# Kernel optimization log

Hardware: AMD Instinct MI355X
Metric: run time of the kernel (lower is better)

Reference implementation:

```python
import jax, jax.numpy as jnp
import numpy as np

B, L, D_MODEL = 4, 2048, 512
N_HEAD, D_K, D_V = 8, 64, 64
RANK = 20


def tt_linear(x, g1, g2, g3, g4, b):
    # TT-matrix linear: input modes (4,4,8,4), output modes (4,4,8,4), ranks [1,20,20,20,1]
    Bx, Lx, _ = x.shape
    t = x.reshape(Bx * Lx, 4, 4, 8, 4)
    t = jnp.einsum('bwxyz,wou->bxyzou', t, g1[0])        # g1: [1,m1,n1,r1]
    t = jnp.einsum('bxyzou,uxpv->byzopv', t, g2)         # g2: [r1,m2,n2,r2]
    t = jnp.einsum('byzopv,vyqw->bzopqw', t, g3)         # g3: [r2,m3,n3,r3]
    t = jnp.einsum('bzopqw,wzs->bopqs', t, g4[..., 0])   # g4: [r3,m4,n4,1]
    return t.reshape(Bx, Lx, -1) + b


def setup_inputs() -> dict:
    key = jax.random.key(0)
    ks = jax.random.split(key, 8)
    scale = jnp.float32(0.15)
    inp = {}
    for name, kk in zip(['wq', 'wk', 'wv', 'fc'], ks[:4]):
        sub = jax.random.split(kk, 4)
        inp[name + '_g1'] = jax.random.normal(sub[0], (1, 4, 4, RANK), jnp.float32) * scale
        inp[name + '_g2'] = jax.random.normal(sub[1], (RANK, 4, 4, RANK), jnp.float32) * scale
        inp[name + '_g3'] = jax.random.normal(sub[2], (RANK, 8, 8, RANK), jnp.float32) * scale
        inp[name + '_g4'] = jax.random.normal(sub[3], (RANK, 4, 4, 1), jnp.float32) * scale
        inp[name + '_b'] = jnp.zeros((D_MODEL,), jnp.float32)
    inp['q'] = jax.random.normal(ks[4], (B, L, D_MODEL), jnp.float32)
    inp['k'] = jax.random.normal(ks[5], (B, L, D_MODEL), jnp.float32)
    inp['v'] = jax.random.normal(ks[6], (B, L, D_MODEL), jnp.float32)
    inp['ln_g'] = jnp.ones((D_MODEL,), jnp.float32)
    inp['ln_b'] = jnp.zeros((D_MODEL,), jnp.float32)
    return inp


def reference(q, k, v,
              wq_g1, wq_g2, wq_g3, wq_g4, wq_b,
              wk_g1, wk_g2, wk_g3, wk_g4, wk_b,
              wv_g1, wv_g2, wv_g3, wv_g4, wv_b,
              fc_g1, fc_g2, fc_g3, fc_g4, fc_b,
              ln_g, ln_b):
    Bx, Lq, _ = q.shape
    residual = q
    qh = tt_linear(q, wq_g1, wq_g2, wq_g3, wq_g4, wq_b).reshape(Bx, Lq, N_HEAD, D_K).transpose(0, 2, 1, 3)
    kh = tt_linear(k, wk_g1, wk_g2, wk_g3, wk_g4, wk_b).reshape(Bx, Lq, N_HEAD, D_K).transpose(0, 2, 1, 3)
    vh = tt_linear(v, wv_g1, wv_g2, wv_g3, wv_g4, wv_b).reshape(Bx, Lq, N_HEAD, D_V).transpose(0, 2, 1, 3)
    temp = jnp.sqrt(jnp.float32(D_K))
    attn = jnp.einsum('bhqd,bhkd->bhqk', qh / temp, kh)  # explicit [B,H,L,L] scores
    attn = jax.nn.softmax(attn, axis=-1)
    o = jnp.einsum('bhqk,bhkd->bhqd', attn, vh)
    o = o.transpose(0, 2, 1, 3).reshape(Bx, Lq, N_HEAD * D_V)
    out = tt_linear(o, fc_g1, fc_g2, fc_g3, fc_g4, fc_b) + residual
    mu = out.mean(-1, keepdims=True)
    var = out.var(-1, keepdims=True)
    out = (out - mu) / jnp.sqrt(var + 1e-12) * ln_g + ln_b
    return (out, attn)
```

## Files before the change

kernel.cpp:

```cpp
#include <hip/hip_runtime.h>
#include <hip/hip_bf16.h>
#include <math.h>

#define BB 4
#define LL 2048
#define DM 512
#define NH 8
#define DK 64
#define RANK 20

typedef __attribute__((ext_vector_type(8))) short short8;
typedef __attribute__((ext_vector_type(4))) short short4b;
typedef __attribute__((ext_vector_type(4))) float f32x4;
typedef __hip_bfloat16 bf16;

__device__ inline short to_bf(float x) {
    bf16 h = __float2bfloat16(x);
    return *reinterpret_cast<short*>(&h);
}
__device__ inline unsigned pk2(float lo, float hi) {
    return ((unsigned)(unsigned short)to_bf(hi) << 16) |
           (unsigned)(unsigned short)to_bf(lo);
}

struct BwArgs {
    const float* g1[4]; const float* g2[4]; const float* g3[4]; const float* g4[4];
    bf16* wt[4];
};
__global__ __launch_bounds__(256) void build_w_kernel(BwArgs args)
{
    int s4 = blockIdx.y;
    const float* __restrict__ g1 = args.g1[s4];
    const float* __restrict__ g2 = args.g2[s4];
    const float* __restrict__ g3 = args.g3[s4];
    const float* __restrict__ g4 = args.g4[s4];
    bf16* __restrict__ Wt = args.wt[s4];

    int idx = blockIdx.x * 256 + threadIdx.x;
    if (idx >= 4*4*8*4*4*8) return;
    int q = idx & 7; int t = idx >> 3;
    int p = t & 3;  t >>= 2;
    int o = t & 3;  t >>= 2;
    int y = t & 7;  t >>= 3;
    int x = t & 3;  t >>= 2;
    int w = t & 3;

    float c[RANK];
    for (int v = 0; v < RANK; ++v) c[v] = 0.f;
    for (int u = 0; u < RANK; ++u) {
        float a = g1[(w*4 + o)*RANK + u];
        const float* g2p = g2 + ((u*4 + x)*4 + p)*RANK;
        for (int v = 0; v < RANK; ++v) c[v] += a * g2p[v];
    }
    float d[RANK];
    for (int r = 0; r < RANK; ++r) d[r] = 0.f;
    for (int v = 0; v < RANK; ++v) {
        float cv = c[v];
        const float* g3p = g3 + ((v*8 + y)*8 + q)*RANK;
        for (int r = 0; r < RANK; ++r) d[r] += cv * g3p[r];
    }
    for (int z = 0; z < 4; ++z) {
        for (int s = 0; s < 4; ++s) {
            float acc = 0.f;
            for (int r = 0; r < RANK; ++r) acc += d[r] * g4[(r*4 + z)*4 + s];
            int i = ((w*4 + x)*8 + y)*4 + z;
            int j = ((o*4 + p)*8 + q)*4 + s;
            Wt[(size_t)j*DM + i] = __float2bfloat16(acc);
        }
    }
}

struct CvtArgs { const float* src[3]; bf16* dst[3]; };
__global__ __launch_bounds__(256) void cvt_kernel(CvtArgs args)
{
    int a = blockIdx.y;
    const float* __restrict__ s = args.src[a];
    bf16* __restrict__ d = args.dst[a];
    size_t i = ((size_t)blockIdx.x * 256 + threadIdx.x) * 16;
    #pragma unroll
    for (int half = 0; half < 2; ++half) {
        float4 v0 = *(const float4*)&s[i + half*8];
        float4 v1 = *(const float4*)&s[i + half*8 + 4];
        short8 h;
        h[0] = to_bf(v0.x); h[1] = to_bf(v0.y); h[2] = to_bf(v0.z); h[3] = to_bf(v0.w);
        h[4] = to_bf(v1.x); h[5] = to_bf(v1.y); h[6] = to_bf(v1.z); h[7] = to_bf(v1.w);
        *(short8*)&d[i + half*8] = h;
    }
}

#define GEMM_CORE128x64(Ap, Bp)                                                    \
    f32x4 acc[4][2] = {};                                                          \
    for (int k0 = 0; k0 < DM; k0 += 32) {                                          \
        short8 a[4], b[2];                                                         \
        _Pragma("unroll")                                                          \
        for (int mt = 0; mt < 4; ++mt)                                             \
            a[mt] = *(const short8*)&Ap[(size_t)(mt*16 + l15)*DM + k0 + l4*8];     \
        _Pragma("unroll")                                                          \
        for (int nt = 0; nt < 2; ++nt)                                             \
            b[nt] = *(const short8*)&Bp[(size_t)(nt*16 + l15)*DM + k0 + l4*8];     \
        _Pragma("unroll")                                                          \
        for (int mt = 0; mt < 4; ++mt)                                             \
            _Pragma("unroll")                                                      \
            for (int nt = 0; nt < 2; ++nt)                                         \
                acc[mt][nt] = __builtin_amdgcn_mfma_f32_16x16x32_bf16(             \
                    a[mt], b[nt], acc[mt][nt], 0, 0, 0);                           \
    }

struct QkvArgs {
    const bf16* A[3]; const bf16* W[3]; const float* bias[3];
    bf16* outQ; bf16* outK; bf16* outV;
};
__global__ __launch_bounds__(256) void gemm_qkv_kernel(QkvArgs args)
{
    int z = blockIdx.z;
    const bf16* __restrict__ A  = args.A[z];
    const bf16* __restrict__ Wt = args.W[z];
    const float* __restrict__ bias = args.bias[z];

    int m0 = blockIdx.x * 128, n0 = blockIdx.y * 64;
    int t = threadIdx.x, lane = t & 63, wave = t >> 6;
    int l15 = lane & 15, l4 = lane >> 4;
    int wm = wave >> 1, wn = wave & 1;
    const bf16* Ap = A  + (size_t)(m0 + wm*64)*DM;
    const bf16* Bp = Wt + (size_t)(n0 + wn*32)*DM;

    GEMM_CORE128x64(Ap, Bp)

    if (z < 2) {
        bf16* __restrict__ out = (z == 0) ? args.outQ : args.outK;
        float oscale = (z == 0) ? 0.18033688f : 1.0f;
        #pragma unroll
        for (int mt = 0; mt < 4; ++mt) {
            #pragma unroll
            for (int r = 0; r < 4; ++r) {
                int m = m0 + wm*64 + mt*16 + l4*4 + r;
                int l = m & (LL-1), bb = m >> 11;
                #pragma unroll
                for (int nt = 0; nt < 2; ++nt) {
                    int n = n0 + wn*32 + nt*16 + l15;
                    int h = n >> 6, d = n & 63;
                    float val = (acc[mt][nt][r] + bias[n]) * oscale;
                    out[(((size_t)(bb*NH + h))*LL + l)*DK + d] = __float2bfloat16(val);
                }
            }
        }
    } else {
        #pragma unroll
        for (int mt = 0; mt < 4; ++mt) {
            int mbase = m0 + wm*64 + mt*16 + l4*4;
            int l = mbase & (LL-1), bb = mbase >> 11;
            #pragma unroll
            for (int nt = 0; nt < 2; ++nt) {
                int n = n0 + wn*32 + nt*16 + l15;
                int h = n >> 6, d = n & 63;
                float bv = bias[n];
                short4b h4;
                #pragma unroll
                for (int r = 0; r < 4; ++r) h4[r] = to_bf(acc[mt][nt][r] + bv);
                *(short4b*)&args.outV[((size_t)(bb*NH + h)*DK + d)*LL + l] = h4;
            }
        }
    }
}

__global__ __launch_bounds__(256) void gemm_fc_kernel(
    const bf16* __restrict__ A, const bf16* __restrict__ Wt,
    const float* __restrict__ bias, float* __restrict__ out)
{
    int m0 = blockIdx.x * 128, n0 = blockIdx.y * 64;
    int t = threadIdx.x, lane = t & 63, wave = t >> 6;
    int l15 = lane & 15, l4 = lane >> 4;
    int wm = wave >> 1, wn = wave & 1;
    const bf16* Ap = A  + (size_t)(m0 + wm*64)*DM;
    const bf16* Bp = Wt + (size_t)(n0 + wn*32)*DM;

    GEMM_CORE128x64(Ap, Bp)

    #pragma unroll
    for (int mt = 0; mt < 4; ++mt) {
        #pragma unroll
        for (int r = 0; r < 4; ++r) {
            int m = m0 + wm*64 + mt*16 + l4*4 + r;
            #pragma unroll
            for (int nt = 0; nt < 2; ++nt) {
                int n = n0 + wn*32 + nt*16 + l15;
                out[(size_t)m*DM + n] = acc[mt][nt][r] + bias[n];
            }
        }
    }
}

__global__ __launch_bounds__(256, 2) void attn_a_kernel(
    const bf16* __restrict__ Qh, const bf16* __restrict__ Kh,
    const bf16* __restrict__ Vt, float* __restrict__ invl_g,
    bf16* __restrict__ O)
{
    __shared__ __align__(16) bf16 Ks[128*64];
    __shared__ __align__(16) bf16 Vs[64*128];
    __shared__ __align__(16) bf16 Ps[4][32*128];
    __shared__ float invlS[4][32];

    int qt = blockIdx.x, bh = blockIdx.y;
    int q0 = qt * 128;
    int t = threadIdx.x, lane = t & 63, wave = t >> 6;
    int l15 = lane & 15, l4 = lane >> 4;
    int qr0 = wave * 32;

    const bf16* Qp = Qh + ((size_t)bh * LL + q0 + qr0) * DK;
    const bf16* Kp = Kh + (size_t)bh * LL * DK;
    const bf16* Vp = Vt + (size_t)bh * DK * LL;

    short8 aq0[2], aq1[2];
    #pragma unroll
    for (int f = 0; f < 2; ++f) {
        aq0[f] = *(const short8*)&Qp[(size_t)(f*16 + l15)*DK + l4*8];
        aq1[f] = *(const short8*)&Qp[(size_t)(f*16 + l15)*DK + 32 + l4*8];
    }

    int srow = t >> 3, sseg = t & 7;
    int swr = (l15 & 7) << 4;

    float lsum[2] = {0.f, 0.f};
    f32x4 o_acc[2][4] = {};

    for (int kc = 0; kc < LL; kc += 128) {
        #pragma unroll
        for (int i = 0; i < 4; ++i) {
            int row = srow + i*32;
            int off = (sseg*16) ^ ((row & 7) << 4);
            *(short8*)&Ks[row*64 + (off >> 1)] =
                *(const short8*)&Kp[(size_t)(kc + row)*DK + sseg*8];
        }
        #pragma unroll
        for (int i = 0; i < 2; ++i) {
            int vrow = (t >> 3) + i*32;
            #pragma unroll
            for (int j = 0; j < 2; ++j) {
                int gran = (t & 7) + j*8;
                int vb = (gran*16) ^ ((vrow & 7) << 4);
                *(short8*)&Vs[vrow*128 + (vb >> 1)] =
                    *(const short8*)&Vp[(size_t)vrow*LL + kc + gran*8];
            }
        }
        __syncthreads();

        #pragma unroll
        for (int ct = 0; ct < 8; ++ct) {
            int rb = (ct*16 + l15) * 64;
            short8 k0f = *(const short8*)&Ks[rb + (((l4*16) ^ swr) >> 1)];
            short8 k1f = *(const short8*)&Ks[rb + (((64 + l4*16) ^ swr) >> 1)];
            #pragma unroll
            for (int f = 0; f < 2; ++f) {
                f32x4 s = {0.f, 0.f, 0.f, 0.f};
                s = __builtin_amdgcn_mfma_f32_16x16x32_bf16(k0f, aq0[f], s, 0, 0, 0);
                s = __builtin_amdgcn_mfma_f32_16x16x32_bf16(k1f, aq1[f], s, 0, 0, 0);
                float p0 = exp2f(s[0]), p1 = exp2f(s[1]);
                float p2 = exp2f(s[2]), p3 = exp2f(s[3]);
                lsum[f] += (p0 + p1) + (p2 + p3);
                uint2 w2;
                w2.x = pk2(p0, p1);
                w2.y = pk2(p2, p3);
                int kb = (ct*32 + l4*8) ^ swr;
                *(uint2*)((char*)&Ps[wave][(f*16 + l15)*128] + kb) = w2;
            }
        }

        #pragma unroll
        for (int f = 0; f < 2; ++f)
            #pragma unroll
            for (int kt = 0; kt < 4; ++kt) {
                short8 a = *(const short8*)
                    &Ps[wave][(f*16 + l15)*128 + (((kt*64 + l4*16) ^ swr) >> 1)];
                #pragma unroll
                for (int dt = 0; dt < 4; ++dt) {
                    short8 b = *(const short8*)
                        &Vs[(dt*16 + l15)*128 + (((kt*64 + l4*16) ^ swr) >> 1)];
                    o_acc[f][dt] = __builtin_amdgcn_mfma_f32_16x16x32_bf16(
                        a, b, o_acc[f][dt], 0, 0, 0);
                }
            }
        __syncthreads();
    }

    #pragma unroll
    for (int f = 0; f < 2; ++f) {
        float ss = lsum[f];
        ss += __shfl_xor(ss, 16);
        ss += __shfl_xor(ss, 32);
        float inv = 1.0f / ss;
        if (l4 == 0) {
            invl_g[(size_t)bh * LL + q0 + qr0 + f*16 + l15] = inv;
            invlS[wave][f*16 + l15] = inv;
        }
    }

    int bb = bh >> 3, h = bh & 7;
    #pragma unroll
    for (int f = 0; f < 2; ++f) {
        f32x4 iv = *(f32x4*)&invlS[wave][f*16 + l4*4];
        #pragma unroll
        for (int dt = 0; dt < 4; ++dt)
            #pragma unroll
            for (int r = 0; r < 4; ++r) {
                int row = q0 + qr0 + f*16 + l4*4 + r;
                O[((size_t)bb * LL + row) * DM + h*DK + dt*16 + l15] =
                    __float2bfloat16(o_acc[f][dt][r] * iv[r]);
            }
    }
}

__global__ __launch_bounds__(256, 4) void attn_p_kernel(
    const bf16* __restrict__ Qh, const bf16* __restrict__ Kh,
    const float* __restrict__ invl_g, float* __restrict__ attn)
{
    __shared__ __align__(16) bf16 Ks[256*64];

    int ko = blockIdx.x, qt = blockIdx.y, bh = blockIdx.z;
    int kc0 = ko * 256, q0 = qt * 128;
    int t = threadIdx.x, lane = t & 63, wave = t >> 6;
    int l15 = lane & 15, l4 = lane >> 4;
    int qr0 = wave * 32;

    const bf16* Qp = Qh + ((size_t)bh * LL + q0 + qr0) * DK;
    const bf16* Kp = Kh + ((size_t)bh * LL + kc0) * DK;

    short8 bq0[2], bq1[2];
    float inv[2];
    #pragma unroll
    for (int f = 0; f < 2; ++f) {
        bq0[f] = *(const short8*)&Qp[(size_t)(f*16 + l15)*DK + l4*8];
        bq1[f] = *(const short8*)&Qp[(size_t)(f*16 + l15)*DK + 32 + l4*8];
        inv[f] = invl_g[(size_t)bh * LL + q0 + qr0 + f*16 + l15];
    }

    #pragma unroll
    for (int g = 0; g < 8; ++g) {
        int off = (g*16) ^ ((t & 7) << 4);
        *(short8*)&Ks[t*64 + (off >> 1)] =
            *(const short8*)&Kp[(size_t)t*DK + g*8];
    }
    __syncthreads();

    int swr = (l15 & 7) << 4;
    float* ap0 = attn + ((size_t)bh * LL + q0 + qr0 + l15) * LL + kc0;
    float* ap1 = ap0 + (size_t)16 * LL;

    #pragma unroll 4
    for (int ct = 0; ct < 16; ++ct) {
        int rb = (ct*16 + l15) * 64;
        short8 a0 = *(const short8*)&Ks[rb + (((l4*16) ^ swr) >> 1)];
        short8 a1 = *(const short8*)&Ks[rb + (((64 + l4*16) ^ swr) >> 1)];
        #pragma unroll
        for (int f = 0; f < 2; ++f) {
            f32x4 s = {0.f, 0.f, 0.f, 0.f};
            s = __builtin_amdgcn_mfma_f32_16x16x32_bf16(a0, bq0[f], s, 0, 0, 0);
            s = __builtin_amdgcn_mfma_f32_16x16x32_bf16(a1, bq1[f], s, 0, 0, 0);
            float4 o;
            o.x = exp2f(s[0]) * inv[f];
            o.y = exp2f(s[1]) * inv[f];
            o.z = exp2f(s[2]) * inv[f];
            o.w = exp2f(s[3]) * inv[f];
            *(float4*)&((f ? ap1 : ap0)[ct*16 + l4*4]) = o;
        }
    }
}

__global__ __launch_bounds__(256) void ln_kernel(
    const float* __restrict__ Y, const float* __restrict__ Res,
    const float* __restrict__ g, const float* __restrict__ bta,
    float* __restrict__ out)
{
    int row = blockIdx.x;
    int t = threadIdx.x;
    const float* yp = Y  + (size_t)row*DM;
    const float* rp = Res + (size_t)row*DM;
    float v0 = yp[t]       + rp[t];
    float v1 = yp[t + 256] + rp[t + 256];
    float s1 = v0 + v1;
    float s2 = v0*v0 + v1*v1;
    __shared__ float red1[4], red2[4];
    #pragma unroll
    for (int off = 32; off >= 1; off >>= 1) {
        s1 += __shfl_xor(s1, off);
        s2 += __shfl_xor(s2, off);
    }
    int w = t >> 6;
    if ((t & 63) == 0) { red1[w] = s1; red2[w] = s2; }
    __syncthreads();
    float mu = (red1[0]+red1[1]+red1[2]+red1[3]) * (1.0f/DM);
    float ms = (red2[0]+red2[1]+red2[2]+red2[3]) * (1.0f/DM);
    float inv = rsqrtf(ms - mu*mu + 1e-12f);
    out[(size_t)row*DM + t]       = (v0 - mu)*inv*g[t]       + bta[t];
    out[(size_t)row*DM + t + 256] = (v1 - mu)*inv*g[t + 256] + bta[t + 256];
}

extern "C" void kernel_launch(void* const* d_in, const int* in_sizes, int n_in,
                              void* d_out, int out_size, void* d_ws, size_t ws_size,
                              hipStream_t stream)
{
    const float* G[4][5];
    for (int s = 0; s < 4; ++s)
        for (int i = 0; i < 5; ++i)
            G[s][i] = (const float*)d_in[s*5 + i];
    const float* q   = (const float*)d_in[20];
    const float* k   = (const float*)d_in[21];
    const float* v   = (const float*)d_in[22];
    const float* lng = (const float*)d_in[23];
    const float* lnb = (const float*)d_in[24];

    float* out  = (float*)d_out;
    float* attn = out + (size_t)BB*LL*DM;

    const size_t NTOK = (size_t)BB*LL*DM;
    bf16* wt  = (bf16*)d_ws;
    bf16* qbf = wt + 4*(size_t)DM*DM;
    bf16* kbf = qbf + NTOK;
    bf16* vbf = kbf + NTOK;
    bf16* qh  = vbf + NTOK;
    bf16* kh  = qh + NTOK;
    bf16* vt  = kh + NTOK;
    bf16* o   = vt + NTOK;
    float* y  = (float*)(o + NTOK);
    float* invl = y + NTOK;

    BwArgs bw;
    for (int s = 0; s < 4; ++s) {
        bw.g1[s] = G[s][0]; bw.g2[s] = G[s][1];
        bw.g3[s] = G[s][2]; bw.g4[s] = G[s][3];
        bw.wt[s] = wt + (size_t)s*DM*DM;
    }
    build_w_kernel<<<dim3(64, 4), 256, 0, stream>>>(bw);

    CvtArgs cv;
    cv.src[0] = q; cv.src[1] = k; cv.src[2] = v;
    cv.dst[0] = qbf; cv.dst[1] = kbf; cv.dst[2] = vbf;
    cvt_kernel<<<dim3(NTOK/(256*16), 3), 256, 0, stream>>>(cv);

    QkvArgs qa;
    qa.A[0] = qbf; qa.A[1] = kbf; qa.A[2] = vbf;
    qa.W[0] = wt; qa.W[1] = wt + (size_t)DM*DM; qa.W[2] = wt + 2*(size_t)DM*DM;
    qa.bias[0] = G[0][4]; qa.bias[1] = G[1][4]; qa.bias[2] = G[2][4];
    qa.outQ = qh; qa.outK = kh; qa.outV = vt;
    gemm_qkv_kernel<<<dim3(BB*LL/128, DM/64, 3), 256, 0, stream>>>(qa);

    attn_a_kernel<<<dim3(LL/128, BB*NH), 256, 0, stream>>>(qh, kh, vt, invl, o);

    attn_p_kernel<<<dim3(LL/256, LL/128, BB*NH), 256, 0, stream>>>(qh, kh, invl, attn);

    gemm_fc_kernel<<<dim3(BB*LL/128, DM/64), 256, 0, stream>>>(
        o, wt + 3*(size_t)DM*DM, G[3][4], y);
    ln_kernel<<<BB*LL, 256, 0, stream>>>(y, q, lng, lnb, out);
}
```

Before: 342.6 us.

## Halve attention P scratch in LDS by staging second tile in registers

The attention kernel now keeps only one 16-row P tile per wave in shared memory. The second tile's probabilities are held in registers and written into the same buffer after the first PV product finishes. This cuts LDS use so three blocks can fit per CU, and launch bounds are raised to match. The trade-off is extra register pressure under a tighter per-thread register budget, and the two PV phases are serialised through the shared buffer.

New measurement: 391.5 us. 1.14x slower.

```diff
diff --git a/kernel.cpp b/kernel.cpp
--- a/kernel.cpp
+++ b/kernel.cpp
@@ -190,14 +190,14 @@
     }
 }
 
-__global__ __launch_bounds__(256, 2) void attn_a_kernel(
+__global__ __launch_bounds__(256, 3) void attn_a_kernel(
     const bf16* __restrict__ Qh, const bf16* __restrict__ Kh,
     const bf16* __restrict__ Vt, float* __restrict__ invl_g,
     bf16* __restrict__ O)
 {
     __shared__ __align__(16) bf16 Ks[128*64];
     __shared__ __align__(16) bf16 Vs[64*128];
-    __shared__ __align__(16) bf16 Ps[4][32*128];
+    __shared__ __align__(16) bf16 Ps[4][16*128];
     __shared__ float invlS[4][32];
 
     int qt = blockIdx.x, bh = blockIdx.y;
@@ -222,6 +222,7 @@
 
     float lsum[2] = {0.f, 0.f};
     f32x4 o_acc[2][4] = {};
+    char* PsRow = (char*)&Ps[wave][l15*128];
 
     for (int kc = 0; kc < LL; kc += 128) {
         #pragma unroll
@@ -244,41 +245,66 @@
         }
         __syncthreads();
 
+        uint2 preg[8];
         #pragma unroll
         for (int ct = 0; ct < 8; ++ct) {
             int rb = (ct*16 + l15) * 64;
             short8 k0f = *(const short8*)&Ks[rb + (((l4*16) ^ swr) >> 1)];
             short8 k1f = *(const short8*)&Ks[rb + (((64 + l4*16) ^ swr) >> 1)];
-            #pragma unroll
-            for (int f = 0; f < 2; ++f) {
+            int kb = (ct*32 + l4*8) ^ swr;
+            {
                 f32x4 s = {0.f, 0.f, 0.f, 0.f};
-                s = __builtin_amdgcn_mfma_f32_16x16x32_bf16(k0f, aq0[f], s, 0, 0, 0);
-                s = __builtin_amdgcn_mfma_f32_16x16x32_bf16(k1f, aq1[f], s, 0, 0, 0);
+                s = __builtin_amdgcn_mfma_f32_16x16x32_bf16(k0f, aq0[0], s, 0, 0, 0);
+                s = __builtin_amdgcn_mfma_f32_16x16x32_bf16(k1f, aq1[0], s, 0, 0, 0);
                 float p0 = exp2f(s[0]), p1 = exp2f(s[1]);
                 float p2 = exp2f(s[2]), p3 = exp2f(s[3]);
-                lsum[f] += (p0 + p1) + (p2 + p3);
-                uint2 w2;
-                w2.x = pk2(p0, p1);
-                w2.y = pk2(p2, p3);
-                int kb = (ct*32 + l4*8) ^ swr;
-                *(uint2*)((char*)&Ps[wave][(f*16 + l15)*128] + kb) = w2;
-            }
-        }
-
-        #pragma unroll
-        for (int f = 0; f < 2; ++f)
-            #pragma unroll
-            for (int kt = 0; kt < 4; ++kt) {
-                short8 a = *(const short8*)
-                    &Ps[wave][(f*16 + l15)*128 + (((kt*64 + l4*16) ^ swr) >> 1)];
-                #pragma unroll
-                for (int dt = 0; dt < 4; ++dt) {
-                    short8 b = *(const short8*)
-                        &Vs[(dt*16 + l15)*128 + (((kt*64 + l4*16) ^ swr) >> 1)];
-                    o_acc[f][dt] = __builtin_amdgcn_mfma_f32_16x16x32_bf16(
-                        a, b, o_acc[f][dt], 0, 0, 0);
-                }
-            }
+                lsum[0] += (p0 + p1) + (p2 + p3);
+                uint2 w2; w2.x = pk2(p0, p1); w2.y = pk2(p2, p3);
+                *(uint2*)(PsRow + kb) = w2;
+            }
+            {
+                f32x4 s = {0.f, 0.f, 0.f, 0.f};
+                s = __builtin_amdgcn_mfma_f32_16x16x32_bf16(k0f, aq0[1], s, 0, 0, 0);
+                s = __builtin_amdgcn_mfma_f32_16x16x32_bf16(k1f, aq1[1], s, 0, 0, 0);
+                float p0 = exp2f(s[0]), p1 = exp2f(s[1]);
+                float p2 = exp2f(s[2]), p3 = exp2f(s[3]);
+                lsum[1] += (p0 + p1) + (p2 + p3);
+                preg[ct].x = pk2(p0, p1);
+                preg[ct].y = pk2(p2, p3);
+            }
+        }
+
+        #pragma unroll
+        for (int kt = 0; kt < 4; ++kt) {
+            short8 a = *(const short8*)
+                &Ps[wave][l15*128 + (((kt*64 + l4*16) ^ swr) >> 1)];
+            #pragma unroll
+            for (int dt = 0; dt < 4; ++dt) {
+                short8 b = *(const short8*)
+                    &Vs[(dt*16 + l15)*128 + (((kt*64 + l4*16) ^ swr) >> 1)];
+                o_acc[0][dt] = __builtin_amdgcn_mfma_f32_16x16x32_bf16(
+                    a, b, o_acc[0][dt], 0, 0, 0);
+            }
+        }
+
+        #pragma unroll
+        for (int ct = 0; ct < 8; ++ct) {
+            int kb = (ct*32 + l4*8) ^ swr;
+            *(uint2*)(PsRow + kb) = preg[ct];
+        }
+
+        #pragma unroll
+        for (int kt = 0; kt < 4; ++kt) {
+            short8 a = *(const short8*)
+                &Ps[wave][l15*128 + (((kt*64 + l4*16) ^ swr) >> 1)];
+            #pragma unroll
+            for (int dt = 0; dt < 4; ++dt) {
+                short8 b = *(const short8*)
+                    &Vs[(dt*16 + l15)*128 + (((kt*64 + l4*16) ^ swr) >> 1)];
+                o_acc[1][dt] = __builtin_amdgcn_mfma_f32_16x16x32_bf16(
+                    a, b, o_acc[1][dt], 0, 0, 0);
+            }
+        }
         __syncthreads();
     }
 
```
